# Kernel optimization log

Measured on AMD Instinct MI355X. Metric: run time of the kernel, lower is better.

The kernel has to match this reference:

```python
import jax, jax.numpy as jnp
import numpy as np

FIELD_DIMS = [100000, 50000, 1000, 500, 100, 50, 20, 10]
INPUT_DIM = sum(FIELD_DIMS)            # 151680
NUM_FIELDS = len(FIELD_DIMS)           # 8
FACTOR_DIM = 16
HIDDEN = [256, 128]
OFFSETS = np.concatenate([[0], np.cumsum(FIELD_DIMS)[:-1]]).astype(np.int32)
BATCH = 2048
EPS = 1e-5


def setup_inputs() -> dict:
    key = jax.random.key(0)
    ks = jax.random.split(key, 32)
    # per-field indices, each within its own cardinality
    x = jnp.stack([
        jax.random.randint(ks[f], (BATCH,), 0, FIELD_DIMS[f], dtype=jnp.int32)
        for f in range(NUM_FIELDS)
    ], axis=1)  # [B, F]
    # concatenated embedding tables (xavier_uniform per torch init, approximated with uniform)
    lim = float(np.sqrt(6.0 / (max(FIELD_DIMS) + FACTOR_DIM)))
    emb_table = jax.random.uniform(ks[8], (INPUT_DIM, FACTOR_DIM), minval=-lim, maxval=lim, dtype=jnp.float32)
    # FM linear: weight ~ N(0, 0.01), bias 0
    w_lin = 0.01 * jax.random.normal(ks[9], (INPUT_DIM,), dtype=jnp.float32)
    b_lin = jnp.zeros((), dtype=jnp.float32)
    d0 = NUM_FIELDS * FACTOR_DIM  # 128
    def lin(k, fan_in, fan_out):
        b = float(np.sqrt(1.0 / fan_in))
        kw, kb = jax.random.split(k)
        W = jax.random.uniform(kw, (fan_in, fan_out), minval=-b, maxval=b, dtype=jnp.float32)
        bias = jax.random.uniform(kb, (fan_out,), minval=-b, maxval=b, dtype=jnp.float32)
        return W, bias
    W1, b1 = lin(ks[10], d0, HIDDEN[0])
    W2, b2 = lin(ks[11], HIDDEN[0], HIDDEN[1])
    W3, b3 = lin(ks[12], HIDDEN[1], 1)
    g1 = jnp.ones((HIDDEN[0],), jnp.float32); be1 = jnp.zeros((HIDDEN[0],), jnp.float32)
    g2 = jnp.ones((HIDDEN[1],), jnp.float32); be2 = jnp.zeros((HIDDEN[1],), jnp.float32)
    return {"x": x, "emb_table": emb_table, "w_lin": w_lin, "b_lin": b_lin,
            "W1": W1, "b1": b1, "g1": g1, "be1": be1,
            "W2": W2, "b2": b2, "g2": g2, "be2": be2,
            "W3": W3, "b3": b3}


def _batchnorm(h, gamma, beta):
    # training-mode BN (torch default): biased batch variance
    m = jnp.mean(h, axis=0)
    v = jnp.mean((h - m) ** 2, axis=0)
    return gamma * (h - m) / jnp.sqrt(v + EPS) + beta


def reference(x, emb_table, w_lin, b_lin, W1, b1, g1, be1, W2, b2, g2, be2, W3, b3):
    B = x.shape[0]
    offsets = jnp.asarray(OFFSETS)
    # --- faithful to original bug: scatter one-hot uses RAW x (no field offsets) ---
    sparse_x = jnp.zeros((B, INPUT_DIM), jnp.float32).at[
        jnp.arange(B)[:, None], x].set(1.0)  # duplicates collapse to 1.0, like scatter_
    y_linear = sparse_x @ w_lin + b_lin  # [B]
    # --- dense field embeddings (offset gather into concatenated table) ---
    dense_x = emb_table[x + offsets[None, :]]  # [B, F, K]
    s = jnp.sum(dense_x, axis=1)               # [B, K]
    square_of_sum = s * s
    sum_of_square = jnp.sum(dense_x * dense_x, axis=1)
    y_pairwise = 0.5 * jnp.sum(square_of_sum - sum_of_square, axis=1)  # [B]
    y_fm = y_linear + y_pairwise
    # --- DNN on concatenated embeddings ---
    h = dense_x.reshape(B, NUM_FIELDS * FACTOR_DIM)
    h = jax.nn.relu(_batchnorm(h @ W1 + b1, g1, be1))
    h = jax.nn.relu(_batchnorm(h @ W2 + b2, g2, be2))
    y_dnn = (h @ W3 + b3)[:, 0]  # [B]
    return y_fm + y_dnn
```

## Files before the change

### kernel.cpp

```cpp
#include <hip/hip_runtime.h>

#define EPS 1e-5f

static __device__ const int OFFS[8] = {0, 100000, 150000, 151000, 151500, 151600, 151650, 151670};

__global__ __launch_bounds__(256) void k1_gather_fm_gemm1(
    const int* __restrict__ x, const float* __restrict__ emb,
    const float* __restrict__ wlin, const float* __restrict__ blin,
    const float* __restrict__ W1, const float* __restrict__ b1,
    float* __restrict__ yfm, float* __restrict__ z1, float* __restrict__ p1)
{
    __shared__ __align__(16) float h0s[16][128];
    __shared__ __align__(16) float red[2][8][128];
    const int t = threadIdx.x;
    const int rt = blockIdx.x >> 1;
    const int ch = blockIdx.x & 1;

    {
        const int g_r = t >> 4, g_l = t & 15;
        const int b = rt * 16 + g_r;
        int idx[8];
#pragma unroll
        for (int f = 0; f < 8; ++f) idx[f] = x[b * 8 + f];

        float s = 0.f, ssq = 0.f;
#pragma unroll
        for (int f = 0; f < 8; ++f) {
            float e = emb[(idx[f] + OFFS[f]) * 16 + g_l];
            h0s[g_r][f * 16 + g_l] = e;
            s += e;
            ssq += e * e;
        }
        if (ch == 0) {
            float pair = s * s - ssq;
#pragma unroll
            for (int m = 8; m >= 1; m >>= 1) pair += __shfl_xor(pair, m);
            if (g_l == 0) {
                float lin = 0.f;
#pragma unroll
                for (int f = 0; f < 8; ++f) {
                    bool dup = false;
                    for (int g = 0; g < f; ++g) dup = dup || (idx[g] == idx[f]);
                    if (!dup) lin += wlin[idx[f]];
                }
                yfm[b] = 0.5f * pair + lin + blin[0];
            }
        }
    }
    __syncthreads();

    const int jg = t & 31, rp = t >> 5;
    const float* Wb = W1 + ch * 128 + jg * 4;
    float acc0[4] = {0.f, 0.f, 0.f, 0.f};
    float acc1[4] = {0.f, 0.f, 0.f, 0.f};
    for (int k = 0; k < 128; k += 4) {
        float4 ha = *(const float4*)&h0s[rp * 2][k];
        float4 hb = *(const float4*)&h0s[rp * 2 + 1][k];
        const float ha_[4] = {ha.x, ha.y, ha.z, ha.w};
        const float hb_[4] = {hb.x, hb.y, hb.z, hb.w};
#pragma unroll
        for (int kk = 0; kk < 4; ++kk) {
            float4 w = *(const float4*)&Wb[(k + kk) * 256];
            acc0[0] += ha_[kk] * w.x; acc0[1] += ha_[kk] * w.y;
            acc0[2] += ha_[kk] * w.z; acc0[3] += ha_[kk] * w.w;
            acc1[0] += hb_[kk] * w.x; acc1[1] += hb_[kk] * w.y;
            acc1[2] += hb_[kk] * w.z; acc1[3] += hb_[kk] * w.w;
        }
    }
    float4 bj = *(const float4*)&b1[ch * 128 + jg * 4];
    const float bj_[4] = {bj.x, bj.y, bj.z, bj.w};
    float zs[4], zss[4];
    float z0[4], z1v[4];
#pragma unroll
    for (int c = 0; c < 4; ++c) {
        z0[c] = acc0[c] + bj_[c];
        z1v[c] = acc1[c] + bj_[c];
        zs[c] = z0[c] + z1v[c];
        zss[c] = z0[c] * z0[c] + z1v[c] * z1v[c];
    }
    const int r0 = rt * 16 + rp * 2;
    *(float4*)&z1[r0 * 256 + ch * 128 + jg * 4] = make_float4(z0[0], z0[1], z0[2], z0[3]);
    *(float4*)&z1[(r0 + 1) * 256 + ch * 128 + jg * 4] = make_float4(z1v[0], z1v[1], z1v[2], z1v[3]);
    *(float4*)&red[0][rp][jg * 4] = make_float4(zs[0], zs[1], zs[2], zs[3]);
    *(float4*)&red[1][rp][jg * 4] = make_float4(zss[0], zss[1], zss[2], zss[3]);
    __syncthreads();
    if (t < 128) {
        float s = 0.f, ss = 0.f;
#pragma unroll
        for (int q = 0; q < 8; ++q) { s += red[0][q][t]; ss += red[1][q][t]; }
        p1[rt * 512 + ch * 128 + t] = s;
        p1[rt * 512 + 256 + ch * 128 + t] = ss;
    }
}

__global__ __launch_bounds__(512) void k2_bn1_gemm2(
    const float* __restrict__ z1, const float* __restrict__ p1,
    const float* __restrict__ g1, const float* __restrict__ be1,
    const float* __restrict__ W2, const float* __restrict__ b2,
    float* __restrict__ z2, float* __restrict__ p2)
{
    __shared__ __align__(16) float h1s[8][256];
    __shared__ __align__(16) float sclS[256], shfS[256];
    __shared__ __align__(16) float sp[2][256], ssp[2][256];
    __shared__ __align__(16) float red2[2][8][128];
    const int t = threadIdx.x, rb = blockIdx.x;

    {
        const int col = t & 255, h = t >> 8;
        float s = 0.f, ss = 0.f;
#pragma unroll 16
        for (int q = h * 64; q < h * 64 + 64; ++q) {
            s += p1[q * 512 + col];
            ss += p1[q * 512 + 256 + col];
        }
        sp[h][col] = s; ssp[h][col] = ss;
    }
    __syncthreads();
    if (t < 256) {
        float s = sp[0][t] + sp[1][t];
        float ss = ssp[0][t] + ssp[1][t];
        float mean = s * (1.f / 2048.f);
        float var = ss * (1.f / 2048.f) - mean * mean;
        float sc = g1[t] * __frsqrt_rn(var + EPS);
        sclS[t] = sc;
        shfS[t] = be1[t] - mean * sc;
    }
    __syncthreads();

    {
        const int lr = t >> 6, lc = (t & 63) * 4;
        float4 zv = *(const float4*)&z1[(rb * 8 + lr) * 256 + lc];
        float4 sc = *(const float4*)&sclS[lc];
        float4 sh = *(const float4*)&shfS[lc];
        float4 hv;
        hv.x = fmaxf(zv.x * sc.x + sh.x, 0.f);
        hv.y = fmaxf(zv.y * sc.y + sh.y, 0.f);
        hv.z = fmaxf(zv.z * sc.z + sh.z, 0.f);
        hv.w = fmaxf(zv.w * sc.w + sh.w, 0.f);
        *(float4*)&h1s[lr][lc] = hv;
    }
    __syncthreads();

    const int r = t >> 6, j2 = (t & 63) * 2;
    float acc[2] = {0.f, 0.f};
    for (int k = 0; k < 256; k += 4) {
        float4 hv = *(const float4*)&h1s[r][k];
        const float h_[4] = {hv.x, hv.y, hv.z, hv.w};
#pragma unroll
        for (int kk = 0; kk < 4; ++kk) {
            float2 w = *(const float2*)&W2[(k + kk) * 128 + j2];
            acc[0] += h_[kk] * w.x;
            acc[1] += h_[kk] * w.y;
        }
    }
    float2 bj = *(const float2*)&b2[j2];
    float za = acc[0] + bj.x, zb = acc[1] + bj.y;
    *(float2*)&z2[(rb * 8 + r) * 128 + j2] = make_float2(za, zb);
    *(float2*)&red2[0][r][j2] = make_float2(za, zb);
    *(float2*)&red2[1][r][j2] = make_float2(za * za, zb * zb);
    __syncthreads();
    if (t < 128) {
        float s = 0.f, ss = 0.f;
#pragma unroll
        for (int q = 0; q < 8; ++q) { s += red2[0][q][t]; ss += red2[1][q][t]; }
        p2[rb * 256 + t] = s;
        p2[rb * 256 + 128 + t] = ss;
    }
}

__global__ __launch_bounds__(256) void k3_bn2_out(
    const float* __restrict__ z2, const float* __restrict__ p2,
    const float* __restrict__ g2, const float* __restrict__ be2,
    const float* __restrict__ W3, const float* __restrict__ b3,
    const float* __restrict__ yfm, float* __restrict__ out)
{
    __shared__ __align__(16) float sp[2][128], ssp[2][128];
    __shared__ __align__(16) float scl[128], shf[128];
    const int t = threadIdx.x, blk = blockIdx.x;
    {
        const int col = t & 127, h = t >> 7;
        float s = 0.f, ss = 0.f;
#pragma unroll 16
        for (int q = h * 128; q < h * 128 + 128; ++q) {
            s += p2[q * 256 + col];
            ss += p2[q * 256 + 128 + col];
        }
        sp[h][col] = s; ssp[h][col] = ss;
    }
    __syncthreads();
    if (t < 128) {
        float s = sp[0][t] + sp[1][t];
        float ss = ssp[0][t] + ssp[1][t];
        float mean = s * (1.f / 2048.f);
        float var = ss * (1.f / 2048.f) - mean * mean;
        float sc = g2[t] * __frsqrt_rn(var + EPS);
        scl[t] = sc;
        shf[t] = be2[t] - mean * sc;
    }
    __syncthreads();

    const int r = t >> 5, l32 = t & 31;
    const int b = blk * 8 + r;
    float4 zv = *(const float4*)&z2[b * 128 + l32 * 4];
    float4 sc = *(const float4*)&scl[l32 * 4];
    float4 sh = *(const float4*)&shf[l32 * 4];
    float4 wv = *(const float4*)&W3[l32 * 4];
    float acc = fmaxf(zv.x * sc.x + sh.x, 0.f) * wv.x
              + fmaxf(zv.y * sc.y + sh.y, 0.f) * wv.y
              + fmaxf(zv.z * sc.z + sh.z, 0.f) * wv.z
              + fmaxf(zv.w * sc.w + sh.w, 0.f) * wv.w;
#pragma unroll
    for (int m = 16; m >= 1; m >>= 1) acc += __shfl_xor(acc, m);
    if (l32 == 0) out[b] = acc + b3[0] + yfm[b];
}

extern "C" void kernel_launch(void* const* d_in, const int* in_sizes, int n_in,
                              void* d_out, int out_size, void* d_ws, size_t ws_size,
                              hipStream_t stream) {
    const int*   x    = (const int*)d_in[0];
    const float* emb  = (const float*)d_in[1];
    const float* wlin = (const float*)d_in[2];
    const float* blin = (const float*)d_in[3];
    const float* W1   = (const float*)d_in[4];
    const float* b1   = (const float*)d_in[5];
    const float* g1   = (const float*)d_in[6];
    const float* be1  = (const float*)d_in[7];
    const float* W2   = (const float*)d_in[8];
    const float* b2   = (const float*)d_in[9];
    const float* g2   = (const float*)d_in[10];
    const float* be2  = (const float*)d_in[11];
    const float* W3   = (const float*)d_in[12];
    const float* b3   = (const float*)d_in[13];

    float* ws  = (float*)d_ws;
    float* yfm = ws;
    float* z1  = yfm + 2048;
    float* p1  = z1 + 2048 * 256;
    float* z2  = p1 + 128 * 512;
    float* p2  = z2 + 2048 * 128;
    float* out = (float*)d_out;

    k1_gather_fm_gemm1<<<256, 256, 0, stream>>>(x, emb, wlin, blin, W1, b1, yfm, z1, p1);
    k2_bn1_gemm2<<<256, 512, 0, stream>>>(z1, p1, g1, be1, W2, b2, z2, p2);
    k3_bn2_out<<<256, 256, 0, stream>>>(z2, p2, g2, be2, W3, b3, yfm, out);
}
```

Measured before the change: 37.84 us.

## Restructure GEMM1 to full-width 8-row tiles and interleave BN partial sums

The first kernel now gives each block 8 rows across all 256 output columns with 512 threads, rather than splitting columns across two blocks of 16 rows. This removes the duplicated embedding gather and lets the FM and linear terms be reduced with wave shuffles. The GEMM loops batch sixteen weight loads ahead of the FMAs to raise memory-level parallelism, at some cost in registers. BN partial sums are stored as interleaved (sum, sumsq) float2 pairs so the later reductions read with float2 loads, but kernel 2 now has twice as many partial rows to reduce (256 instead of 128), and each W1 row is read by every block.

```diff
diff --git a/kernel.cpp b/kernel.cpp
--- a/kernel.cpp
+++ b/kernel.cpp
@@ -4,92 +4,81 @@
 
 static __device__ const int OFFS[8] = {0, 100000, 150000, 151000, 151500, 151600, 151650, 151670};
 
-__global__ __launch_bounds__(256) void k1_gather_fm_gemm1(
+__global__ __launch_bounds__(512) void k1_gather_fm_gemm1(
     const int* __restrict__ x, const float* __restrict__ emb,
     const float* __restrict__ wlin, const float* __restrict__ blin,
     const float* __restrict__ W1, const float* __restrict__ b1,
     float* __restrict__ yfm, float* __restrict__ z1, float* __restrict__ p1)
 {
-    __shared__ __align__(16) float h0s[16][128];
-    __shared__ __align__(16) float red[2][8][128];
-    const int t = threadIdx.x;
-    const int rt = blockIdx.x >> 1;
-    const int ch = blockIdx.x & 1;
-
-    {
-        const int g_r = t >> 4, g_l = t & 15;
-        const int b = rt * 16 + g_r;
-        int idx[8];
-#pragma unroll
-        for (int f = 0; f < 8; ++f) idx[f] = x[b * 8 + f];
-
-        float s = 0.f, ssq = 0.f;
-#pragma unroll
-        for (int f = 0; f < 8; ++f) {
-            float e = emb[(idx[f] + OFFS[f]) * 16 + g_l];
-            h0s[g_r][f * 16 + g_l] = e;
-            s += e;
-            ssq += e * e;
-        }
-        if (ch == 0) {
-            float pair = s * s - ssq;
-#pragma unroll
-            for (int m = 8; m >= 1; m >>= 1) pair += __shfl_xor(pair, m);
-            if (g_l == 0) {
-                float lin = 0.f;
-#pragma unroll
-                for (int f = 0; f < 8; ++f) {
-                    bool dup = false;
-                    for (int g = 0; g < f; ++g) dup = dup || (idx[g] == idx[f]);
-                    if (!dup) lin += wlin[idx[f]];
-                }
-                yfm[b] = 0.5f * pair + lin + blin[0];
-            }
-        }
-    }
-    __syncthreads();
-
-    const int jg = t & 31, rp = t >> 5;
-    const float* Wb = W1 + ch * 128 + jg * 4;
-    float acc0[4] = {0.f, 0.f, 0.f, 0.f};
-    float acc1[4] = {0.f, 0.f, 0.f, 0.f};
-    for (int k = 0; k < 128; k += 4) {
-        float4 ha = *(const float4*)&h0s[rp * 2][k];
-        float4 hb = *(const float4*)&h0s[rp * 2 + 1][k];
-        const float ha_[4] = {ha.x, ha.y, ha.z, ha.w};
-        const float hb_[4] = {hb.x, hb.y, hb.z, hb.w};
-#pragma unroll
-        for (int kk = 0; kk < 4; ++kk) {
-            float4 w = *(const float4*)&Wb[(k + kk) * 256];
-            acc0[0] += ha_[kk] * w.x; acc0[1] += ha_[kk] * w.y;
-            acc0[2] += ha_[kk] * w.z; acc0[3] += ha_[kk] * w.w;
-            acc1[0] += hb_[kk] * w.x; acc1[1] += hb_[kk] * w.y;
-            acc1[2] += hb_[kk] * w.z; acc1[3] += hb_[kk] * w.w;
-        }
-    }
-    float4 bj = *(const float4*)&b1[ch * 128 + jg * 4];
-    const float bj_[4] = {bj.x, bj.y, bj.z, bj.w};
-    float zs[4], zss[4];
-    float z0[4], z1v[4];
-#pragma unroll
-    for (int c = 0; c < 4; ++c) {
-        z0[c] = acc0[c] + bj_[c];
-        z1v[c] = acc1[c] + bj_[c];
-        zs[c] = z0[c] + z1v[c];
-        zss[c] = z0[c] * z0[c] + z1v[c] * z1v[c];
-    }
-    const int r0 = rt * 16 + rp * 2;
-    *(float4*)&z1[r0 * 256 + ch * 128 + jg * 4] = make_float4(z0[0], z0[1], z0[2], z0[3]);
-    *(float4*)&z1[(r0 + 1) * 256 + ch * 128 + jg * 4] = make_float4(z1v[0], z1v[1], z1v[2], z1v[3]);
-    *(float4*)&red[0][rp][jg * 4] = make_float4(zs[0], zs[1], zs[2], zs[3]);
-    *(float4*)&red[1][rp][jg * 4] = make_float4(zss[0], zss[1], zss[2], zss[3]);
-    __syncthreads();
-    if (t < 128) {
-        float s = 0.f, ss = 0.f;
-#pragma unroll
-        for (int q = 0; q < 8; ++q) { s += red[0][q][t]; ss += red[1][q][t]; }
-        p1[rt * 512 + ch * 128 + t] = s;
-        p1[rt * 512 + 256 + ch * 128 + t] = ss;
+    __shared__ __align__(16) float h0s[8][128];
+    __shared__ __align__(16) float redS[8][256];
+    __shared__ __align__(16) float redQ[8][256];
+
+    const int t = threadIdx.x, blk = blockIdx.x;
+    const int r = t >> 6, c = t & 63;
+    const int row = blk * 8 + r;
+
+    {
+        const int f = c >> 3, dp = c & 7;
+        const int idxf = x[row * 8 + f];
+        float2 e = *(const float2*)&emb[(size_t)(idxf + OFFS[f]) * 16 + dp * 2];
+        *(float2*)&h0s[r][f * 16 + dp * 2] = e;
+
+        float sx = e.x, sy = e.y, qx = e.x * e.x, qy = e.y * e.y;
+#pragma unroll
+        for (int m = 8; m <= 32; m <<= 1) {
+            sx += __shfl_xor(sx, m); sy += __shfl_xor(sy, m);
+            qx += __shfl_xor(qx, m); qy += __shfl_xor(qy, m);
+        }
+        float pair = (sx * sx - qx) + (sy * sy - qy);
+        pair += __shfl_xor(pair, 1);
+        pair += __shfl_xor(pair, 2);
+        pair += __shfl_xor(pair, 4);
+
+        float lin = 0.f;
+        if (c < 8) {
+            int ids[8];
+#pragma unroll
+            for (int g = 0; g < 8; ++g) ids[g] = x[row * 8 + g];
+            bool dup = false;
+            for (int g = 0; g < c; ++g) dup = dup || (ids[g] == ids[c]);
+            lin = dup ? 0.f : wlin[ids[c]];
+        }
+        lin += __shfl_xor(lin, 1);
+        lin += __shfl_xor(lin, 2);
+        lin += __shfl_xor(lin, 4);
+        if (c == 0) yfm[row] = 0.5f * pair + lin + blin[0];
+    }
+    __syncthreads();
+
+    const int j0 = c * 4;
+    float a0 = 0.f, a1 = 0.f, a2 = 0.f, a3 = 0.f;
+#pragma unroll
+    for (int k0 = 0; k0 < 128; k0 += 16) {
+        float4 h[4];
+#pragma unroll
+        for (int i = 0; i < 4; ++i) h[i] = *(const float4*)&h0s[r][k0 + i * 4];
+        float4 w[16];
+#pragma unroll
+        for (int kk = 0; kk < 16; ++kk) w[kk] = *(const float4*)&W1[(size_t)(k0 + kk) * 256 + j0];
+#pragma unroll
+        for (int kk = 0; kk < 16; ++kk) {
+            const float hv = ((const float*)h)[kk];
+            a0 += hv * w[kk].x; a1 += hv * w[kk].y;
+            a2 += hv * w[kk].z; a3 += hv * w[kk].w;
+        }
+    }
+    float4 b4 = *(const float4*)&b1[j0];
+    float4 zv = make_float4(a0 + b4.x, a1 + b4.y, a2 + b4.z, a3 + b4.w);
+    *(float4*)&z1[(size_t)row * 256 + j0] = zv;
+    *(float4*)&redS[r][j0] = zv;
+    *(float4*)&redQ[r][j0] = make_float4(zv.x * zv.x, zv.y * zv.y, zv.z * zv.z, zv.w * zv.w);
+    __syncthreads();
+    if (t < 256) {
+        float s = 0.f, q = 0.f;
+#pragma unroll
+        for (int rr = 0; rr < 8; ++rr) { s += redS[rr][t]; q += redQ[rr][t]; }
+        *(float2*)&p1[(size_t)(blk * 256 + t) * 2] = make_float2(s, q);
     }
 }
 
@@ -101,26 +90,28 @@
 {
     __shared__ __align__(16) float h1s[8][256];
     __shared__ __align__(16) float sclS[256], shfS[256];
-    __shared__ __align__(16) float sp[2][256], ssp[2][256];
-    __shared__ __align__(16) float red2[2][8][128];
-    const int t = threadIdx.x, rb = blockIdx.x;
+    __shared__ __align__(16) float sbuf[2][256], qbuf[2][256];
+    __shared__ __align__(16) float redS[8][128];
+    __shared__ __align__(16) float redQ[8][128];
+
+    const int t = threadIdx.x, blk = blockIdx.x;
 
     {
         const int col = t & 255, h = t >> 8;
-        float s = 0.f, ss = 0.f;
+        float s = 0.f, q = 0.f;
 #pragma unroll 16
-        for (int q = h * 64; q < h * 64 + 64; ++q) {
-            s += p1[q * 512 + col];
-            ss += p1[q * 512 + 256 + col];
-        }
-        sp[h][col] = s; ssp[h][col] = ss;
+        for (int i = 0; i < 128; ++i) {
+            float2 v = *(const float2*)&p1[(size_t)((h * 128 + i) * 256 + col) * 2];
+            s += v.x; q += v.y;
+        }
+        sbuf[h][col] = s; qbuf[h][col] = q;
     }
     __syncthreads();
     if (t < 256) {
-        float s = sp[0][t] + sp[1][t];
-        float ss = ssp[0][t] + ssp[1][t];
+        float s = sbuf[0][t] + sbuf[1][t];
+        float q = qbuf[0][t] + qbuf[1][t];
         float mean = s * (1.f / 2048.f);
-        float var = ss * (1.f / 2048.f) - mean * mean;
+        float var  = q * (1.f / 2048.f) - mean * mean;
         float sc = g1[t] * __frsqrt_rn(var + EPS);
         sclS[t] = sc;
         shfS[t] = be1[t] - mean * sc;
@@ -129,7 +120,7 @@
 
     {
         const int lr = t >> 6, lc = (t & 63) * 4;
-        float4 zv = *(const float4*)&z1[(rb * 8 + lr) * 256 + lc];
+        float4 zv = *(const float4*)&z1[(size_t)(blk * 8 + lr) * 256 + lc];
         float4 sc = *(const float4*)&sclS[lc];
         float4 sh = *(const float4*)&shfS[lc];
         float4 hv;
@@ -141,30 +132,34 @@
     }
     __syncthreads();
 
-    const int r = t >> 6, j2 = (t & 63) * 2;
-    float acc[2] = {0.f, 0.f};
-    for (int k = 0; k < 256; k += 4) {
-        float4 hv = *(const float4*)&h1s[r][k];
-        const float h_[4] = {hv.x, hv.y, hv.z, hv.w};
-#pragma unroll
-        for (int kk = 0; kk < 4; ++kk) {
-            float2 w = *(const float2*)&W2[(k + kk) * 128 + j2];
-            acc[0] += h_[kk] * w.x;
-            acc[1] += h_[kk] * w.y;
-        }
-    }
-    float2 bj = *(const float2*)&b2[j2];
-    float za = acc[0] + bj.x, zb = acc[1] + bj.y;
-    *(float2*)&z2[(rb * 8 + r) * 128 + j2] = make_float2(za, zb);
-    *(float2*)&red2[0][r][j2] = make_float2(za, zb);
-    *(float2*)&red2[1][r][j2] = make_float2(za * za, zb * zb);
+    const int r = t >> 6, j0 = (t & 63) * 2;
+    float a0 = 0.f, a1 = 0.f;
+#pragma unroll
+    for (int k0 = 0; k0 < 256; k0 += 16) {
+        float4 h[4];
+#pragma unroll
+        for (int i = 0; i < 4; ++i) h[i] = *(const float4*)&h1s[r][k0 + i * 4];
+        float2 w[16];
+#pragma unroll
+        for (int kk = 0; kk < 16; ++kk) w[kk] = *(const float2*)&W2[(size_t)(k0 + kk) * 128 + j0];
+#pragma unroll
+        for (int kk = 0; kk < 16; ++kk) {
+            const float hv = ((const float*)h)[kk];
+            a0 += hv * w[kk].x; a1 += hv * w[kk].y;
+        }
+    }
+    float2 b2v = *(const float2*)&b2[j0];
+    float za = a0 + b2v.x, zb = a1 + b2v.y;
+    const int row = blk * 8 + r;
+    *(float2*)&z2[(size_t)row * 128 + j0] = make_float2(za, zb);
+    *(float2*)&redS[r][j0] = make_float2(za, zb);
+    *(float2*)&redQ[r][j0] = make_float2(za * za, zb * zb);
     __syncthreads();
     if (t < 128) {
-        float s = 0.f, ss = 0.f;
-#pragma unroll
-        for (int q = 0; q < 8; ++q) { s += red2[0][q][t]; ss += red2[1][q][t]; }
-        p2[rb * 256 + t] = s;
-        p2[rb * 256 + 128 + t] = ss;
+        float s = 0.f, q = 0.f;
+#pragma unroll
+        for (int rr = 0; rr < 8; ++rr) { s += redS[rr][t]; q += redQ[rr][t]; }
+        *(float2*)&p2[(size_t)(blk * 128 + t) * 2] = make_float2(s, q);
     }
 }
 
@@ -174,44 +169,46 @@
     const float* __restrict__ W3, const float* __restrict__ b3,
     const float* __restrict__ yfm, float* __restrict__ out)
 {
-    __shared__ __align__(16) float sp[2][128], ssp[2][128];
+    __shared__ __align__(16) float sbuf[2][128], qbuf[2][128];
     __shared__ __align__(16) float scl[128], shf[128];
+
     const int t = threadIdx.x, blk = blockIdx.x;
+
     {
         const int col = t & 127, h = t >> 7;
-        float s = 0.f, ss = 0.f;
+        float s = 0.f, q = 0.f;
 #pragma unroll 16
-        for (int q = h * 128; q < h * 128 + 128; ++q) {
-            s += p2[q * 256 + col];
-            ss += p2[q * 256 + 128 + col];
-        }
-        sp[h][col] = s; ssp[h][col] = ss;
+        for (int i = 0; i < 128; ++i) {
+            float2 v = *(const float2*)&p2[(size_t)((h * 128 + i) * 128 + col) * 2];
+            s += v.x; q += v.y;
+        }
+        sbuf[h][col] = s; qbuf[h][col] = q;
     }
     __syncthreads();
     if (t < 128) {
-        float s = sp[0][t] + sp[1][t];
-        float ss = ssp[0][t] + ssp[1][t];
+        float s = sbuf[0][t] + sbuf[1][t];
+        float q = qbuf[0][t] + qbuf[1][t];
         float mean = s * (1.f / 2048.f);
-        float var = ss * (1.f / 2048.f) - mean * mean;
+        float var  = q * (1.f / 2048.f) - mean * mean;
         float sc = g2[t] * __frsqrt_rn(var + EPS);
         scl[t] = sc;
         shf[t] = be2[t] - mean * sc;
     }
     __syncthreads();
 
-    const int r = t >> 5, l32 = t & 31;
+    const int r = t >> 5, l = t & 31;
     const int b = blk * 8 + r;
-    float4 zv = *(const float4*)&z2[b * 128 + l32 * 4];
-    float4 sc = *(const float4*)&scl[l32 * 4];
-    float4 sh = *(const float4*)&shf[l32 * 4];
-    float4 wv = *(const float4*)&W3[l32 * 4];
+    float4 zv = *(const float4*)&z2[(size_t)b * 128 + l * 4];
+    float4 sc = *(const float4*)&scl[l * 4];
+    float4 sh = *(const float4*)&shf[l * 4];
+    float4 wv = *(const float4*)&W3[l * 4];
     float acc = fmaxf(zv.x * sc.x + sh.x, 0.f) * wv.x
               + fmaxf(zv.y * sc.y + sh.y, 0.f) * wv.y
               + fmaxf(zv.z * sc.z + sh.z, 0.f) * wv.z
               + fmaxf(zv.w * sc.w + sh.w, 0.f) * wv.w;
 #pragma unroll
     for (int m = 16; m >= 1; m >>= 1) acc += __shfl_xor(acc, m);
-    if (l32 == 0) out[b] = acc + b3[0] + yfm[b];
+    if (l == 0) out[b] = acc + b3[0] + yfm[b];
 }
 
 extern "C" void kernel_launch(void* const* d_in, const int* in_sizes, int n_in,
@@ -236,11 +233,11 @@
     float* yfm = ws;
     float* z1  = yfm + 2048;
     float* p1  = z1 + 2048 * 256;
-    float* z2  = p1 + 128 * 512;
+    float* z2  = p1 + 2 * 256 * 256;
     float* p2  = z2 + 2048 * 128;
     float* out = (float*)d_out;
 
-    k1_gather_fm_gemm1<<<256, 256, 0, stream>>>(x, emb, wlin, blin, W1, b1, yfm, z1, p1);
+    k1_gather_fm_gemm1<<<256, 512, 0, stream>>>(x, emb, wlin, blin, W1, b1, yfm, z1, p1);
     k2_bn1_gemm2<<<256, 512, 0, stream>>>(z1, p1, g1, be1, W2, b2, z2, p2);
     k3_bn2_out<<<256, 256, 0, stream>>>(z2, p2, g2, be2, W3, b3, yfm, out);
 }
```

New measurement: 48.57 us. +28.4%, slower.
